# Performance work log

Hardware: AMD Instinct MI355X
Metric: run time of the kernel (lower is better)

Reference implementation:

```python
import jax, jax.numpy as jnp
import numpy as np

B, L, D, NLAYERS, MAX_NODES, DEG = 32, 512, 768, 3, 128, 8


def _build_graph():
    rng = np.random.default_rng(0)
    per = rng.integers(-32, 33, size=B // 2)
    sizes = np.concatenate([96 + per, 96 - per]).astype(np.int64)  # sum = 96*B = 3072, each in [64,128]
    N = int(sizes.sum())
    offs = np.concatenate([[0], np.cumsum(sizes)])
    batch = np.repeat(np.arange(B), sizes).astype(np.int64)
    pad_idx = np.zeros((B, MAX_NODES), np.int64)
    pad_mask = np.zeros((B, MAX_NODES), bool)
    src, dst = [], []
    for b in range(B):
        n = int(sizes[b])
        pad_idx[b, :n] = np.arange(offs[b], offs[b] + n)
        pad_mask[b, :n] = True
        src.append(rng.integers(offs[b], offs[b] + n, n * DEG))
        dst.append(rng.integers(offs[b], offs[b] + n, n * DEG))
    return N, batch, pad_idx, pad_mask, np.concatenate(src), np.concatenate(dst)


def setup_inputs() -> dict:
    N, batch, pad_idx, pad_mask, esrc, edst = _build_graph()
    key = jax.random.key(0)
    ks = jax.random.split(key, 8)
    s = 1.0 / np.sqrt(D)
    return {
        "x": jax.random.normal(ks[0], (N, D), jnp.float32),
        "text": jax.random.normal(ks[1], (B, L, D), jnp.float32),
        "batch_ent1_d_mask": jnp.ones((B, 1), jnp.float32),
        "batch_ent1_g_mask": jnp.ones((B, 1), jnp.float32),
        "gnn_ws": jax.random.normal(ks[2], (NLAYERS, D, D), jnp.float32) * s,
        "gnn_wn": jax.random.normal(ks[3], (NLAYERS, D, D), jnp.float32) * s,
        "gnn_b": jnp.zeros((NLAYERS, D), jnp.float32),
        "atom_w": jax.random.normal(ks[4], (D, D), jnp.float32) * s,
        "atom_b": jnp.zeros((D,), jnp.float32),
        "rand_emb": jax.random.normal(ks[5], (1, D), jnp.float32),
        "batch": jnp.asarray(batch),
        "pad_idx": jnp.asarray(pad_idx),
        "pad_mask": jnp.asarray(pad_mask),
        "edge_src": jnp.asarray(esrc),
        "edge_dst": jnp.asarray(edst),
    }


def reference(x, text, batch_ent1_d_mask, batch_ent1_g_mask, gnn_ws, gnn_wn, gnn_b,
              atom_w, atom_b, rand_emb, batch, pad_idx, pad_mask, edge_src, edge_dst):
    N = x.shape[0]
    E = edge_src.shape[0]
    maskf = pad_mask.astype(x.dtype)            # [B, M]
    n_per = maskf.sum(axis=1)                   # [B] num real nodes per graph
    # edge-neighbor mean counts (constants w.r.t. x)
    cnt = jax.ops.segment_sum(jnp.ones((E,), x.dtype), edge_dst, num_segments=N)
    inv_cnt = 1.0 / jnp.maximum(cnt, 1.0)
    cms = []
    for i in range(NLAYERS):
        # MoleGraphConv stand-in: mean neighbor aggregation + self transform
        msg = jax.ops.segment_sum(x[edge_src], edge_dst, num_segments=N) * inv_cnt[:, None]
        x = jax.nn.relu(x @ gnn_ws[i] + msg @ gnn_wn[i] + gnn_b[i])
        # ragged gather into padded [B, M, D]
        xp = x[pad_idx] * maskf[..., None]
        # graph -> text cross attention (softmax over text tokens; no mask needed)
        g2t = jax.nn.softmax(jnp.einsum('bmd,bld->bml', xp, text), axis=-1)
        g2t_out = jnp.einsum('bml,bld->bmd', g2t, text)            # [B, M, D]
        # text -> graph cross attention (mask padded nodes)
        t2g_logits = jnp.einsum('bld,bmd->blm', text, xp)
        t2g_logits = jnp.where(pad_mask[:, None, :], t2g_logits, jnp.float32(-1e9))
        t2g = jax.nn.softmax(t2g_logits, axis=-1)
        t2g_out = jnp.einsum('blm,bmd->bld', t2g, xp)              # [B, L, D]
        # mean over concatenated rows [n_i + L] per graph (pool_type=2)
        pooled = ((g2t_out * maskf[..., None]).sum(axis=1) + t2g_out.sum(axis=1)) \
                 / (n_per + jnp.float32(L))[:, None]
        cms.append(pooled)
    out_cms = jnp.mean(jnp.stack(cms, axis=1), axis=1)              # mean over layers
    out_t = text[:, 0, :]
    # scatter-mean of final node features per graph
    gsum = jax.ops.segment_sum(x, batch, num_segments=B)
    gcnt = jax.ops.segment_sum(jnp.ones((N,), x.dtype), batch, num_segments=B)
    xg = gsum / jnp.maximum(gcnt, 1.0)[:, None]
    # dropout is a no-op in eval mode
    out_g = jnp.tanh(xg @ atom_w + atom_b)
    z = rand_emb[0]
    dg = batch_ent1_d_mask * batch_ent1_g_mask
    return jnp.concatenate([
        out_t * batch_ent1_d_mask + (1 - batch_ent1_d_mask) * z,
        out_g * batch_ent1_g_mask + (1 - batch_ent1_g_mask) * z,
        out_cms * dg + (1 - dg) * z,
    ], axis=-1)
```

## Files before the change

### kernel.cpp

```cpp
#include <hip/hip_runtime.h>

#define D 768
#define B 32
#define L 512
#define M 128
#define NNODES 3072
#define NEDGES 24576

using bf16x8 = __attribute__((ext_vector_type(8))) short;
using f32x4  = __attribute__((ext_vector_type(4))) float;

__device__ __forceinline__ float bf2f(unsigned short u) {
  union { unsigned int i; float f; } v; v.i = ((unsigned int)u) << 16; return v.f;
}
__device__ __forceinline__ unsigned short f2bf(float f) {
  union { float f; unsigned int i; } v; v.f = f;
  unsigned int x = v.i;
  return (unsigned short)((x + 0x7FFFu + ((x >> 16) & 1u)) >> 16);
}
__device__ __forceinline__ float ldf(const void* p, size_t i, int f32) {
  return f32 ? ((const float*)p)[i] : bf2f(((const unsigned short*)p)[i]);
}
__device__ __forceinline__ int ldi(const void* p, size_t i, int w64) {
  return w64 ? (int)((const long long*)p)[i] : ((const int*)p)[i];
}
__device__ __forceinline__ f32x4 mfma16(bf16x8 a, bf16x8 b, f32x4 c) {
  return __builtin_amdgcn_mfma_f32_16x16x32_bf16(a, b, c, 0, 0, 0);
}
__device__ __forceinline__ void gl_lds(const unsigned short* gsrc, unsigned short* lbase,
                                       int lane) {
  __builtin_amdgcn_global_load_lds(
      (const __attribute__((address_space(1))) unsigned int*)(gsrc + lane * 8),
      (__attribute__((address_space(3))) unsigned int*)lbase, 16, 0, 0);
}

__device__ __forceinline__ float pk_read(const unsigned short* P, int p, int l, int d) {
  return bf2f(P[(((size_t)(p * 24 + (d >> 5))) << 9) + ((((d & 31) >> 3) << 4) + l) * 8 + (d & 7)]);
}


__global__ void k_init(int* cnt, int* cursor, int* gcnt, float* pooled,
                       const unsigned short* __restrict__ t,
                       const unsigned int* __restrict__ e, int* __restrict__ flags) {
  int i = blockIdx.x * 256 + threadIdx.x;
  if (i < NNODES) { cnt[i] = 0; cursor[i] = 0; }
  if (i < B) gcnt[i] = 0;
  if (i < B * D) pooled[i] = 0.f;
  if (blockIdx.x == 0) {
    __shared__ int r0[256];
    __shared__ unsigned r1[256];
    int tid = threadIdx.x;
    int bad = 0;
    for (int j = tid; j < 8192; j += 256) {
      unsigned short u = t[2 * j];
      unsigned ex = (u >> 7) & 0xFF;
      if (ex >= 0xC0) bad = 1;
    }
    unsigned o = 0;
    for (int j = tid; j < NEDGES / 2; j += 256) o |= e[2 * j + 1];
    r0[tid] = bad; r1[tid] = o;
    __syncthreads();
    for (int s = 128; s > 0; s >>= 1) {
      if (tid < s) { r0[tid] |= r0[tid + s]; r1[tid] |= r1[tid + s]; }
      __syncthreads();
    }
    if (tid == 0) { flags[0] = r0[0]; flags[1] = (r1[0] == 0) ? 1 : 0; }
  }
}

__global__ __launch_bounds__(256) void k_pack_in(
    const void* __restrict__ x_in, unsigned short* __restrict__ x0,
    unsigned short* __restrict__ PkA, const void* __restrict__ text,
    unsigned short* __restrict__ Tpk, const int* __restrict__ flags) {
  __shared__ unsigned short buf[12288];
  int f = flags[0];
  int bid = blockIdx.x, tid = threadIdx.x;
  const void* src; unsigned short* dst; unsigned short* rows; int p;
  if (bid < NNODES / 16) { src = x_in; dst = PkA; rows = x0; p = bid; }
  else                   { src = text; dst = Tpk; rows = nullptr; p = bid - NNODES / 16; }
#pragma unroll
  for (int j = 0; j < 6; ++j) {
    int idx = j * 256 + tid;
    int r = idx / 96, c = idx % 96;
    size_t sbase = (size_t)(p * 16 + r) * 768 + c * 8;
    union { unsigned short v[8]; uint4 q; } u;
    if (f) {
      const float* sp = (const float*)src + sbase;
#pragma unroll
      for (int e = 0; e < 8; ++e) u.v[e] = f2bf(sp[e]);
    } else {
      const unsigned short* sp = (const unsigned short*)src + sbase;
#pragma unroll
      for (int e = 0; e < 8; ++e) u.v[e] = sp[e];
    }
    if (rows) *(uint4*)&rows[sbase] = u.q;
    int lpos = (c >> 2) * 64 + (c & 3) * 16 + r;
#pragma unroll
    for (int e = 0; e < 8; ++e) buf[lpos * 8 + e] = u.v[e];
  }
  __syncthreads();
  uint4* d4 = (uint4*)(dst + (size_t)p * 12288);
  const uint4* b4 = (const uint4*)buf;
#pragma unroll
  for (int j = 0; j < 6; ++j) d4[j * 256 + tid] = b4[j * 256 + tid];
}

__global__ __launch_bounds__(256) void k_pack(const unsigned short* __restrict__ src,
                                              unsigned short* __restrict__ dst) {
  __shared__ unsigned short buf[12288];
  int p = blockIdx.x, tid = threadIdx.x;
#pragma unroll
  for (int j = 0; j < 6; ++j) {
    int idx = j * 256 + tid;
    int r = idx / 96, c = idx % 96;
    size_t sbase = (size_t)(p * 16 + r) * 768 + c * 8;
    uint4 q = *(const uint4*)(src + sbase);
    int lpos = (c >> 2) * 64 + (c & 3) * 16 + r;
    *(uint4*)&buf[lpos * 8] = q;
  }
  __syncthreads();
  uint4* d4 = (uint4*)(dst + (size_t)p * 12288);
  const uint4* b4 = (const uint4*)buf;
#pragma unroll
  for (int j = 0; j < 6; ++j) d4[j * 256 + tid] = b4[j * 256 + tid];
}

__global__ void k_count(const void* __restrict__ edst, const void* __restrict__ batch,
                        const int* __restrict__ flags, int* __restrict__ cnt,
                        int* __restrict__ gcnt) {
  int w = flags[1];
  int i = blockIdx.x * 256 + threadIdx.x;
  if (i < NEDGES) atomicAdd(&cnt[ldi(edst, i, w)], 1);
  if (i < NNODES) atomicAdd(&gcnt[ldi(batch, i, w)], 1);
}

__global__ void k_scan(const int* __restrict__ cnt, int* __restrict__ rowstart) {
  __shared__ int a[NNODES], b[NNODES];
  int tid = threadIdx.x;
  for (int i = tid; i < NNODES; i += 1024) a[i] = cnt[i];
  __syncthreads();
  int* s = a; int* d = b;
  for (int off = 1; off < NNODES; off <<= 1) {
    for (int i = tid; i < NNODES; i += 1024)
      d[i] = s[i] + (i >= off ? s[i - off] : 0);
    __syncthreads();
    int* t = s; s = d; d = t;
  }
  for (int i = tid; i < NNODES; i += 1024) rowstart[i + 1] = s[i];
  if (tid == 0) rowstart[0] = 0;
}

__global__ void k_scatter(const void* __restrict__ esrc, const void* __restrict__ edst,
                          const int* __restrict__ flags, const int* __restrict__ rowstart,
                          int* __restrict__ cursor, int* __restrict__ csr) {
  int w = flags[1];
  int i = blockIdx.x * 256 + threadIdx.x;
  if (i < NEDGES) {
    int dd = ldi(edst, i, w);
    int pos = atomicAdd(&cursor[dd], 1);
    csr[rowstart[dd] + pos] = ldi(esrc, i, w);
  }
}

__global__ void k_transpose(const void* __restrict__ Ws, const void* __restrict__ Wn,
                            const void* __restrict__ Aw, const int* __restrict__ flags,
                            unsigned short* __restrict__ WsT,
                            unsigned short* __restrict__ WnT,
                            unsigned short* __restrict__ AwT) {
  __shared__ unsigned short tile[32][33];
  int f = flags[0];
  int z = blockIdx.z;
  const void* src; unsigned short* dst; size_t zoff;
  if (z < 3)      { src = Ws; zoff = (size_t)z * D * D;       dst = WsT + zoff; }
  else if (z < 6) { src = Wn; zoff = (size_t)(z - 3) * D * D; dst = WnT + zoff; }
  else            { src = Aw; zoff = 0;                       dst = AwT; }
  int k0 = blockIdx.x * 32, n0 = blockIdx.y * 32;
  int tx = threadIdx.x, ty = threadIdx.y;
#pragma unroll
  for (int j = 0; j < 4; ++j)
    tile[ty + j * 8][tx] = f2bf(ldf(src, zoff + (size_t)(k0 + ty + j * 8) * D + n0 + tx, f));
  __syncthreads();
#pragma unroll
  for (int j = 0; j < 4; ++j)
    dst[(size_t)(n0 + ty + j * 8) * D + k0 + tx] = tile[tx][ty + j * 8];
}

__global__ __launch_bounds__(256) void k_packw(
    const unsigned short* __restrict__ WsT, const unsigned short* __restrict__ WnT,
    const unsigned short* __restrict__ AwT, unsigned short* __restrict__ WsPk,
    unsigned short* __restrict__ WnPk, unsigned short* __restrict__ AwPk) {
  __shared__ unsigned short buf[12288];
  int z = blockIdx.y;
  const unsigned short* src; unsigned short* dst;
  if (z < 3)      { src = WsT + (size_t)z * D * D;       dst = WsPk + (size_t)z * D * D; }
  else if (z < 6) { src = WnT + (size_t)(z - 3) * D * D; dst = WnPk + (size_t)(z - 3) * D * D; }
  else            { src = AwT;                           dst = AwPk; }
  int p = blockIdx.x, tid = threadIdx.x;
#pragma unroll
  for (int j = 0; j < 6; ++j) {
    int idx = j * 256 + tid;
    int r = idx / 96, c = idx % 96;
    size_t sbase = (size_t)(p * 16 + r) * 768 + c * 8;
    uint4 q = *(const uint4*)(src + sbase);
    int lpos = (c >> 2) * 64 + (c & 3) * 16 + r;
    *(uint4*)&buf[lpos * 8] = q;
  }
  __syncthreads();
  uint4* d4 = (uint4*)(dst + (size_t)p * 12288);
  const uint4* b4 = (const uint4*)buf;
#pragma unroll
  for (int j = 0; j < 6; ++j) d4[j * 256 + tid] = b4[j * 256 + tid];
}


__global__ __launch_bounds__(256) void k_msg_pack(
    const unsigned short* __restrict__ x, const int* __restrict__ cnt,
    const int* __restrict__ rowstart, const int* __restrict__ csr,
    unsigned short* __restrict__ Mpk) {
  __shared__ unsigned short buf[12288];
  int p = blockIdx.x, tid = threadIdx.x;
  int w = tid >> 6, lane = tid & 63;
#pragma unroll
  for (int i = 0; i < 4; ++i) {
    int r = w * 4 + i;
    int n = p * 16 + r;
    int deg = cnt[n], base = rowstart[n];
    float inv = 1.0f / (float)(deg > 1 ? deg : 1);
    float a[12];
#pragma unroll
    for (int j = 0; j < 12; ++j) a[j] = 0.f;
    for (int e = 0; e < deg; ++e) {
      const uint2* xr = (const uint2*)(x + (size_t)csr[base + e] * D);
#pragma unroll
      for (int j = 0; j < 3; ++j) {
        uint2 v = xr[lane + j * 64];
        a[j * 4 + 0] += bf2f((unsigned short)(v.x & 0xFFFFu));
        a[j * 4 + 1] += bf2f((unsigned short)(v.x >> 16));
        a[j * 4 + 2] += bf2f((unsigned short)(v.y & 0xFFFFu));
        a[j * 4 + 3] += bf2f((unsigned short)(v.y >> 16));
      }
    }
#pragma unroll
    for (int j = 0; j < 3; ++j) {
      int d0 = (lane + j * 64) * 4;
      int c = d0 >> 3, e0 = d0 & 7;
      int lpos = (c >> 2) * 64 + (c & 3) * 16 + r;
      unsigned short* bp = &buf[lpos * 8 + e0];
      bp[0] = f2bf(a[j * 4 + 0] * inv);
      bp[1] = f2bf(a[j * 4 + 1] * inv);
      bp[2] = f2bf(a[j * 4 + 2] * inv);
      bp[3] = f2bf(a[j * 4 + 3] * inv);
    }
  }
  __syncthreads();
  uint4* d4 = (uint4*)(Mpk + (size_t)p * 12288);
  const uint4* b4 = (const uint4*)buf;
#pragma unroll
  for (int j = 0; j < 6; ++j) d4[j * 256 + tid] = b4[j * 256 + tid];
}

__global__ __launch_bounds__(256) void k_gemm_gnn(
    const unsigned short* __restrict__ Xpk, const unsigned short* __restrict__ Mpk,
    const unsigned short* __restrict__ WsPk, const unsigned short* __restrict__ WnPk,
    const void* __restrict__ bias, size_t bias_off, const int* __restrict__ flags,
    unsigned short* __restrict__ Y) {
  __shared__ __align__(16) unsigned short lds[2][4096];
  int f = flags[0];
  int tid = threadIdx.x;
  int wave = tid >> 6, lane = tid & 63;
  int q = lane >> 4, t = lane & 15;
  int wm = wave >> 1, wn = wave & 1;
  int pa = blockIdx.x * 4, pb = blockIdx.y * 4;
  f32x4 acc[2][2];
#pragma unroll
  for (int mi = 0; mi < 2; ++mi)
#pragma unroll
    for (int ni = 0; ni < 2; ++ni)
      acc[mi][ni] = (f32x4){0.f, 0.f, 0.f, 0.f};

  int c0 = wave * 2;
  for (int r = 0; r < 24; ++r) {
    int s0 = r * 2;
    int h = (s0 < 24) ? 0 : 1;
    int kk0 = s0 - h * 24;
    const unsigned short* P = (wave < 2) ? (h ? Mpk : Xpk) : (h ? WnPk : WsPk);
    int pan0 = (wave < 2) ? (pa + c0) : (pb + c0 - 4);
    gl_lds(P + (((size_t)(pan0 * 24 + kk0)) << 9), &lds[0][c0 * 512], lane);
    gl_lds(P + (((size_t)((pan0 + 1) * 24 + kk0)) << 9), &lds[0][(c0 + 1) * 512], lane);
    gl_lds(P + (((size_t)(pan0 * 24 + kk0 + 1)) << 9), &lds[1][c0 * 512], lane);
    gl_lds(P + (((size_t)((pan0 + 1) * 24 + kk0 + 1)) << 9), &lds[1][(c0 + 1) * 512], lane);
    __syncthreads();
#pragma unroll
    for (int st = 0; st < 2; ++st) {
      bf16x8 a0 = *(const bf16x8*)&lds[st][(wm * 2 + 0) * 512 + lane * 8];
      bf16x8 a1 = *(const bf16x8*)&lds[st][(wm * 2 + 1) * 512 + lane * 8];
      bf16x8 b0 = *(const bf16x8*)&lds[st][(4 + wn * 2 + 0) * 512 + lane * 8];
      bf16x8 b1 = *(const bf16x8*)&lds[st][(4 + wn * 2 + 1) * 512 + lane * 8];
      acc[0][0] = mfma16(a0, b0, acc[0][0]);
      acc[0][1] = mfma16(a0, b1, acc[0][1]);
      acc[1][0] = mfma16(a1, b0, acc[1][0]);
      acc[1][1] = mfma16(a1, b1, acc[1][1]);
    }
    __syncthreads();
  }

#pragma unroll
  for (int ni = 0; ni < 2; ++ni) {
    int col = blockIdx.y * 64 + wn * 32 + ni * 16 + t;
    float bv = ldf(bias, bias_off + col, f);
#pragma unroll
    for (int mi = 0; mi < 2; ++mi) {
#pragma unroll
      for (int r = 0; r < 4; ++r) {
        int row = blockIdx.x * 64 + wm * 32 + mi * 16 + q * 4 + r;
        float v = acc[mi][ni][r] + bv;
        Y[(size_t)row * D + col] = f2bf(v > 0.f ? v : 0.f);
      }
    }
  }
}

__global__ __launch_bounds__(256) void k_xp_pack(
    const unsigned short* __restrict__ Xn, const void* __restrict__ pidx,
    const int* __restrict__ flags, const int* __restrict__ gcnt,
    unsigned short* __restrict__ xp, unsigned short* __restrict__ XpPk) {
  __shared__ unsigned short rows[16 * 776];
  int p = blockIdx.x, tid = threadIdx.x;
  int w64 = flags[1];
  int r = tid >> 4, c16 = tid & 15;
  int bm = p * 16 + r;
  int b = bm >> 7, m = bm & 127;
  int nb = gcnt[b];
  uint4* dl = (uint4*)&rows[r * 776];
  if (m < nb) {
    const uint4* srcr = (const uint4*)(Xn + (size_t)ldi(pidx, bm, w64) * D);
#pragma unroll
    for (int j = 0; j < 6; ++j) dl[c16 + j * 16] = srcr[c16 + j * 16];
  } else {
    uint4 z = {0u, 0u, 0u, 0u};
#pragma unroll
    for (int j = 0; j < 6; ++j) dl[c16 + j * 16] = z;
  }
  __syncthreads();
#pragma unroll
  for (int j = 0; j < 6; ++j) {
    int idx = j * 256 + tid;
    int rr = idx / 96, cc = idx % 96;
    uint4 vv = *(const uint4*)&rows[rr * 776 + cc * 8];
    *(uint4*)&xp[(size_t)(p * 16 + rr) * D + cc * 8] = vv;
  }
  unsigned short* pb = XpPk + (size_t)p * 12288;
#pragma unroll
  for (int j = 0; j < 6; ++j) {
    int odx = j * 256 + tid;
    int kk = odx >> 6, lanep = odx & 63;
    int rr = lanep & 15, cg = lanep >> 4;
    int cc = kk * 4 + cg;
    uint4 vv = *(const uint4*)&rows[rr * 776 + cc * 8];
    *(uint4*)&pb[odx * 8] = vv;
  }
}

__global__ __launch_bounds__(256) void k_scores(
    const unsigned short* __restrict__ XpPk, const unsigned short* __restrict__ Tpk,
    float* __restrict__ S) {
  __shared__ __align__(16) unsigned short lds[2][4096];
  int b = blockIdx.z;
  int tid = threadIdx.x;
  int wave = tid >> 6, lane = tid & 63;
  int q = lane >> 4, t = lane & 15;
  int wm = wave >> 1, wn = wave & 1;
  int pa = b * 8 + blockIdx.x * 4;
  int pb = b * 32 + blockIdx.y * 4;
  f32x4 acc[2][2];
#pragma unroll
  for (int mi = 0; mi < 2; ++mi)
#pragma unroll
    for (int ni = 0; ni < 2; ++ni)
      acc[mi][ni] = (f32x4){0.f, 0.f, 0.f, 0.f};

  int c0 = wave * 2;
  const unsigned short* P = (wave < 2) ? XpPk : Tpk;
  int pan0 = (wave < 2) ? (pa + c0) : (pb + c0 - 4);
  for (int r = 0; r < 12; ++r) {
    int s0 = r * 2;
    gl_lds(P + (((size_t)(pan0 * 24 + s0)) << 9), &lds[0][c0 * 512], lane);
    gl_lds(P + (((size_t)((pan0 + 1) * 24 + s0)) << 9), &lds[0][(c0 + 1) * 512], lane);
    gl_lds(P + (((size_t)(pan0 * 24 + s0 + 1)) << 9), &lds[1][c0 * 512], lane);
    gl_lds(P + (((size_t)((pan0 + 1) * 24 + s0 + 1)) << 9), &lds[1][(c0 + 1) * 512], lane);
    __syncthreads();
#pragma unroll
    for (int st = 0; st < 2; ++st) {
      bf16x8 a0 = *(const bf16x8*)&lds[st][(wm * 2 + 0) * 512 + lane * 8];
      bf16x8 a1 = *(const bf16x8*)&lds[st][(wm * 2 + 1) * 512 + lane * 8];
      bf16x8 b0 = *(const bf16x8*)&lds[st][(4 + wn * 2 + 0) * 512 + lane * 8];
      bf16x8 b1 = *(const bf16x8*)&lds[st][(4 + wn * 2 + 1) * 512 + lane * 8];
      acc[0][0] = mfma16(a0, b0, acc[0][0]);
      acc[0][1] = mfma16(a0, b1, acc[0][1]);
      acc[1][0] = mfma16(a1, b0, acc[1][0]);
      acc[1][1] = mfma16(a1, b1, acc[1][1]);
    }
    __syncthreads();
  }

  float* Sb = S + (size_t)b * M * L;
#pragma unroll
  for (int ni = 0; ni < 2; ++ni) {
    int col = blockIdx.y * 64 + wn * 32 + ni * 16 + t;
#pragma unroll
    for (int mi = 0; mi < 2; ++mi) {
#pragma unroll
      for (int r = 0; r < 4; ++r) {
        int row = blockIdx.x * 64 + wm * 32 + mi * 16 + q * 4 + r;
        Sb[(size_t)row * L + col] = acc[mi][ni][r];
      }
    }
  }
}

__global__ __launch_bounds__(256) void k_stats(
    const float* __restrict__ S, const int* __restrict__ gcnt,
    float* __restrict__ rmax, float* __restrict__ rsum,
    float* __restrict__ cmaxv, float* __restrict__ csumv) {
  int bid = blockIdx.x, tid = threadIdx.x;
  if (bid < B * M) {
    __shared__ float red[4];
    int lane = tid & 63, wv = tid >> 6;
    const float* r = S + (size_t)bid * L;
    float s0 = r[tid], s1 = r[tid + 256];
    float m = fmaxf(s0, s1);
#pragma unroll
    for (int o = 32; o > 0; o >>= 1) m = fmaxf(m, __shfl_down(m, o));
    if (lane == 0) red[wv] = m;
    __syncthreads();
    float bm = fmaxf(fmaxf(red[0], red[1]), fmaxf(red[2], red[3]));
    __syncthreads();
    float e = __expf(s0 - bm) + __expf(s1 - bm);
#pragma unroll
    for (int o = 32; o > 0; o >>= 1) e += __shfl_down(e, o);
    if (lane == 0) red[wv] = e;
    __syncthreads();
    if (tid == 0) { rmax[bid] = bm; rsum[bid] = red[0] + red[1] + red[2] + red[3]; }
  } else {
    __shared__ float pm[4][64], ps[4][64];
    int cid = bid - B * M;
    int b = cid >> 3, ly = cid & 7;
    int w = tid >> 6, lane = tid & 63;
    int l = ly * 64 + lane;
    int nb = gcnt[b];
    const float* Sb = S + (size_t)b * M * L;
    int m0 = w * 32, m1 = min(m0 + 32, nb);
    float cm = -1e30f, cs = 0.f;
    for (int m = m0; m < m1; ++m) {
      float s = Sb[(size_t)m * L + l];
      if (s > cm) { cs = cs * __expf(cm - s) + 1.f; cm = s; }
      else cs += __expf(s - cm);
    }
    pm[w][lane] = cm; ps[w][lane] = cs;
    __syncthreads();
    if (w == 0) {
      float CM = -1e30f;
#pragma unroll
      for (int j = 0; j < 4; ++j) CM = fmaxf(CM, pm[j][lane]);
      float CS = 0.f;
#pragma unroll
      for (int j = 0; j < 4; ++j) CS += ps[j][lane] * __expf(pm[j][lane] - CM);
      cmaxv[b * L + l] = CM; csumv[b * L + l] = CS;
    }
  }
}

__global__ __launch_bounds__(256) void k_cross(
    const float* __restrict__ S, const float* __restrict__ rmax,
    const float* __restrict__ rsum, const float* __restrict__ cmaxv,
    const float* __restrict__ csumv, const int* __restrict__ gcnt,
    float* __restrict__ wv, float* __restrict__ t2gcol) {
  int bid = blockIdx.x, tid = threadIdx.x;
  if (bid < 256) {
    __shared__ float rm[M], ri[M];
    __shared__ float pw[4][64];
    int b = bid >> 3, ly = bid & 7;
    int w = tid >> 6, lane = tid & 63;
    if (tid < M) { rm[tid] = rmax[b * M + tid]; ri[tid] = 1.f / rsum[b * M + tid]; }
    __syncthreads();
    int l = ly * 64 + lane;
    int nb = gcnt[b];
    const float* Sb = S + (size_t)b * M * L;
    int m0 = w * 32, m1 = min(m0 + 32, nb);
    float wp = 0.f;
    for (int m = m0; m < m1; ++m)
      wp += __expf(Sb[(size_t)m * L + l] - rm[m]) * ri[m];
    pw[w][lane] = wp;
    __syncthreads();
    if (w == 0)
      wv[b * L + l] = pw[0][lane] + pw[1][lane] + pw[2][lane] + pw[3][lane];
  } else {
    __shared__ float red[4];
    int bm = bid - 256;
    int b = bm >> 7, m = bm & 127;
    int lane = tid & 63, w = tid >> 6;
    int nb = gcnt[b];
    float acc = 0.f;
    if (m < nb) {
      const float* r = S + (size_t)bm * L;
      const float* cm = cmaxv + b * L;
      const float* cs = csumv + b * L;
      acc = __expf(r[tid] - cm[tid]) / cs[tid]
          + __expf(r[tid + 256] - cm[tid + 256]) / cs[tid + 256];
    }
#pragma unroll
    for (int o = 32; o > 0; o >>= 1) acc += __shfl_down(acc, o);
    if (lane == 0) red[w] = acc;
    __syncthreads();
    if (tid == 0) t2gcol[bm] = red[0] + red[1] + red[2] + red[3];
  }
}

__global__ __launch_bounds__(256) void k_pooled(
    const float* __restrict__ wv, const float* __restrict__ t2gcol,
    const unsigned short* __restrict__ Tpk, const unsigned short* __restrict__ xp,
    const int* __restrict__ gcnt, float* __restrict__ pooled) {
  int b = blockIdx.x;
  int d = blockIdx.y * 256 + threadIdx.x;
  int c = blockIdx.z;
  float acc = 0.f;
  if (c < 8) {
    int l0 = c * 64;
    for (int l = l0; l < l0 + 64; ++l) {
      int p = b * 32 + (l >> 4);
      acc += wv[b * L + l] * pk_read(Tpk, p, l & 15, d);
    }
  } else {
    const unsigned short* Xb = xp + (size_t)b * M * D;
    int mm0 = (c - 8) * 64;
    for (int m = mm0; m < mm0 + 64; ++m) acc += t2gcol[b * M + m] * bf2f(Xb[(size_t)m * D + d]);
  }
  atomicAdd(&pooled[(size_t)b * D + d], acc / ((float)gcnt[b] + 512.f));
}


__global__ __launch_bounds__(256) void k_xg(const unsigned short* __restrict__ xp,
                                            const int* __restrict__ gcnt,
                                            unsigned short* __restrict__ xgb) {
  int b = blockIdx.x;
  int d = blockIdx.y * 256 + threadIdx.x;
  int nb = gcnt[b];
  float inv = 1.0f / (float)(nb > 1 ? nb : 1);
  const unsigned short* Xb = xp + (size_t)b * M * D;
  float s = 0.f;
  for (int m = 0; m < M; ++m) s += bf2f(Xb[(size_t)m * D + d]);
  xgb[(size_t)b * D + d] = f2bf(s * inv);
}

__global__ __launch_bounds__(256) void k_atom(const unsigned short* __restrict__ xgb,
                                              const unsigned short* __restrict__ AwPk,
                                              float* __restrict__ gpre) {
  int tid = threadIdx.x;
  int w = tid >> 6, lane = tid & 63;
  int q = lane >> 4, t = lane & 15;
  int nbase = blockIdx.x * 64 + w * 16;
  int pb = nbase >> 4;
  f32x4 acc[2];
  acc[0] = (f32x4){0.f, 0.f, 0.f, 0.f};
  acc[1] = (f32x4){0.f, 0.f, 0.f, 0.f};
  for (int kk = 0; kk < 24; ++kk) {
    bf16x8 a0 = *(const bf16x8*)(xgb + (size_t)t * D + kk * 32 + q * 8);
    bf16x8 a1 = *(const bf16x8*)(xgb + (size_t)(16 + t) * D + kk * 32 + q * 8);
    bf16x8 bv = *(const bf16x8*)(AwPk + (((size_t)(pb * 24 + kk)) << 9) + (lane << 3));
    acc[0] = mfma16(a0, bv, acc[0]);
    acc[1] = mfma16(a1, bv, acc[1]);
  }
#pragma unroll
  for (int mi = 0; mi < 2; ++mi)
#pragma unroll
    for (int r = 0; r < 4; ++r) {
      int row = mi * 16 + q * 4 + r;
      gpre[(size_t)row * D + nbase + t] = acc[mi][r];
    }
}

__global__ __launch_bounds__(256) void k_final(
    const unsigned short* __restrict__ Tpk, const float* __restrict__ gpre,
    const float* __restrict__ pooled, const void* __restrict__ ab,
    const void* __restrict__ dmask, const void* __restrict__ gmask,
    const void* __restrict__ remb, const int* __restrict__ flags,
    void* __restrict__ out) {
  int f = flags[0];
  int b = blockIdx.x, tid = threadIdx.x;
  float dm = ldf(dmask, b, f);
  float gm = ldf(gmask, b, f);
  float dg = dm * gm;
  size_t base = (size_t)b * 2304;
#pragma unroll
  for (int j = 0; j < 3; ++j) {
    int d = tid + j * 256;
    float z = ldf(remb, d, f);
    float tv = pk_read(Tpk, b * 32, 0, d);
    float o0 = tv * dm + (1.f - dm) * z;
    float gv = tanhf(gpre[(size_t)b * D + d] + ldf(ab, d, f));
    float o1 = gv * gm + (1.f - gm) * z;
    float p = pooled[(size_t)b * D + d] * (1.f / 3.f);
    float o2 = p * dg + (1.f - dg) * z;
    if (f) {
      float* of = (float*)out;
      of[base + d] = o0; of[base + 768 + d] = o1; of[base + 1536 + d] = o2;
    } else {
      unsigned short* ob = (unsigned short*)out;
      ob[base + d] = f2bf(o0); ob[base + 768 + d] = f2bf(o1); ob[base + 1536 + d] = f2bf(o2);
    }
  }
}

extern "C" void kernel_launch(void* const* d_in, const int* in_sizes, int n_in,
                              void* d_out, int out_size, void* d_ws, size_t ws_size,
                              hipStream_t stream) {
  const void* x_in  = d_in[0];
  const void* text  = d_in[1];
  const void* dmask = d_in[2];
  const void* gmask = d_in[3];
  const void* gws   = d_in[4];
  const void* gwn   = d_in[5];
  const void* gb    = d_in[6];
  const void* aw    = d_in[7];
  const void* ab    = d_in[8];
  const void* remb  = d_in[9];
  const void* batch = d_in[10];
  const void* pidx  = d_in[11];
  const void* esrc  = d_in[13];
  const void* edst  = d_in[14];

  char* wsp = (char*)d_ws;
  size_t off = 0;
  auto carve = [&](size_t bytes) -> void* {
    void* p = wsp + off;
    off += (bytes + 255) & ~(size_t)255;
    return p;
  };
  int* flags = (int*)carve(2 * 4);
  unsigned short* x0    = (unsigned short*)carve((size_t)NNODES * D * 2);
  unsigned short* xA    = (unsigned short*)carve((size_t)NNODES * D * 2);
  unsigned short* xB    = (unsigned short*)carve((size_t)NNODES * D * 2);
  unsigned short* PkA   = (unsigned short*)carve((size_t)NNODES * D * 2);
  unsigned short* PkB   = (unsigned short*)carve((size_t)NNODES * D * 2);
  unsigned short* Mpk   = (unsigned short*)carve((size_t)NNODES * D * 2);
  unsigned short* Tpk   = (unsigned short*)carve((size_t)B * L * D * 2);
  unsigned short* WsT   = (unsigned short*)carve((size_t)3 * D * D * 2);
  unsigned short* WnT   = (unsigned short*)carve((size_t)3 * D * D * 2);
  unsigned short* AwT   = (unsigned short*)carve((size_t)D * D * 2);
  unsigned short* WsPk  = (unsigned short*)carve((size_t)3 * D * D * 2);
  unsigned short* WnPk  = (unsigned short*)carve((size_t)3 * D * D * 2);
  unsigned short* AwPk  = (unsigned short*)carve((size_t)D * D * 2);
  unsigned short* xp    = (unsigned short*)carve((size_t)B * M * D * 2);
  unsigned short* XpPk  = (unsigned short*)carve((size_t)B * M * D * 2);
  unsigned short* xgb   = (unsigned short*)carve((size_t)B * D * 2);
  float* gpre    = (float*)carve((size_t)B * D * 4);
  float* S       = (float*)carve((size_t)B * M * L * 4);
  float* rmax    = (float*)carve((size_t)B * M * 4);
  float* rsum    = (float*)carve((size_t)B * M * 4);
  float* wv      = (float*)carve((size_t)B * L * 4);
  float* cmaxv   = (float*)carve((size_t)B * L * 4);
  float* csumv   = (float*)carve((size_t)B * L * 4);
  float* t2gcol  = (float*)carve((size_t)B * M * 4);
  float* pooled  = (float*)carve((size_t)B * D * 4);
  int* cnt      = (int*)carve((size_t)NNODES * 4);
  int* rowstart = (int*)carve((size_t)(NNODES + 1) * 4);
  int* cursor   = (int*)carve((size_t)NNODES * 4);
  int* gcnt     = (int*)carve((size_t)B * 4);
  int* csr      = (int*)carve((size_t)NEDGES * 4);

  k_init<<<96, 256, 0, stream>>>(cnt, cursor, gcnt, pooled,
                                 (const unsigned short*)text, (const unsigned int*)edst, flags);
  k_pack_in<<<NNODES / 16 + B * L / 16, 256, 0, stream>>>(x_in, x0, PkA, text, Tpk, flags);
  k_transpose<<<dim3(24, 24, 7), dim3(32, 8), 0, stream>>>(gws, gwn, aw, flags, WsT, WnT, AwT);
  k_packw<<<dim3(48, 7), 256, 0, stream>>>(WsT, WnT, AwT, WsPk, WnPk, AwPk);
  k_count<<<96, 256, 0, stream>>>(edst, batch, flags, cnt, gcnt);
  k_scan<<<1, 1024, 0, stream>>>(cnt, rowstart);
  k_scatter<<<96, 256, 0, stream>>>(esrc, edst, flags, rowstart, cursor, csr);

  const unsigned short* xsrc = x0;
  const unsigned short* Apk = PkA;
  unsigned short* Y[3]   = {xA, xB, xA};
  unsigned short* Npk[3] = {PkB, PkA, nullptr};
  for (int i = 0; i < 3; ++i) {
    k_msg_pack<<<NNODES / 16, 256, 0, stream>>>(xsrc, cnt, rowstart, csr, Mpk);
    k_gemm_gnn<<<dim3(48, 12), 256, 0, stream>>>(Apk, Mpk, WsPk + (size_t)i * D * D,
                                                 WnPk + (size_t)i * D * D, gb, (size_t)i * D,
                                                 flags, Y[i]);
    if (i < 2) k_pack<<<NNODES / 16, 256, 0, stream>>>(Y[i], Npk[i]);
    k_xp_pack<<<B * M / 16, 256, 0, stream>>>(Y[i], pidx, flags, gcnt, xp, XpPk);
    k_scores<<<dim3(2, 8, B), 256, 0, stream>>>(XpPk, Tpk, S);
    k_stats<<<B * M + 256, 256, 0, stream>>>(S, gcnt, rmax, rsum, cmaxv, csumv);
    k_cross<<<256 + B * M, 256, 0, stream>>>(S, rmax, rsum, cmaxv, csumv, gcnt, wv, t2gcol);
    k_pooled<<<dim3(B, 3, 10), 256, 0, stream>>>(wv, t2gcol, Tpk, xp, gcnt, pooled);
    xsrc = Y[i];
    Apk = Npk[i];
  }
  k_xg<<<dim3(B, 3), 256, 0, stream>>>(xp, gcnt, xgb);
  k_atom<<<12, 256, 0, stream>>>(xgb, AwPk, gpre);
  k_final<<<B, 256, 0, stream>>>(Tpk, gpre, pooled, ab, dmask, gmask, remb, flags, d_out);
}
```

Measured before the change: 487.5 us.

## Fuse weight transpose+pack, deepen GEMM K-staging, fold graph mean into xp_pack

```diff
diff --git a/kernel.cpp b/kernel.cpp
--- a/kernel.cpp
+++ b/kernel.cpp
@@ -39,13 +39,13 @@
 }
 
 
-__global__ void k_init(int* cnt, int* cursor, int* gcnt, float* pooled,
+__global__ void k_init(int* cnt, int* cursor, int* gcnt, float* pooled, float* xgacc,
                        const unsigned short* __restrict__ t,
                        const unsigned int* __restrict__ e, int* __restrict__ flags) {
   int i = blockIdx.x * 256 + threadIdx.x;
   if (i < NNODES) { cnt[i] = 0; cursor[i] = 0; }
   if (i < B) gcnt[i] = 0;
-  if (i < B * D) pooled[i] = 0.f;
+  if (i < B * D) { pooled[i] = 0.f; xgacc[i] = 0.f; }
   if (blockIdx.x == 0) {
     __shared__ int r0[256];
     __shared__ unsigned r1[256];
@@ -125,6 +125,46 @@
   for (int j = 0; j < 6; ++j) d4[j * 256 + tid] = b4[j * 256 + tid];
 }
 
+__global__ __launch_bounds__(256) void k_wpack(
+    const void* __restrict__ Ws, const void* __restrict__ Wn, const void* __restrict__ Aw,
+    const int* __restrict__ flags, unsigned short* __restrict__ WsPk,
+    unsigned short* __restrict__ WnPk, unsigned short* __restrict__ AwPk) {
+  __shared__ unsigned short buf[2048];
+  int f = flags[0];
+  int z = blockIdx.z;
+  const void* src; unsigned short* dst; size_t zoff;
+  if (z < 3)      { src = Ws; zoff = (size_t)z * D * D;       dst = WsPk + zoff; }
+  else if (z < 6) { src = Wn; zoff = (size_t)(z - 3) * D * D; dst = WnPk + zoff; }
+  else            { src = Aw; zoff = 0;                       dst = AwPk; }
+  int n0 = blockIdx.x * 64, kk = blockIdx.y;
+  int tid = threadIdx.x;
+  int kl = tid >> 3, c8 = tid & 7;
+  size_t sbase = zoff + (size_t)(kk * 32 + kl) * D + n0 + c8 * 8;
+  unsigned short v[8];
+  if (f) {
+    const float* sp = (const float*)src + sbase;
+#pragma unroll
+    for (int e = 0; e < 8; ++e) v[e] = f2bf(sp[e]);
+  } else {
+    const unsigned short* sp = (const unsigned short*)src + sbase;
+#pragma unroll
+    for (int e = 0; e < 8; ++e) v[e] = sp[e];
+  }
+  int ebit = kl & 7, quad = kl >> 3;
+#pragma unroll
+  for (int i = 0; i < 8; ++i) {
+    int nl = c8 * 8 + i;
+    int pl = nl >> 4;
+    int lane = quad * 16 + (nl & 15);
+    buf[pl * 512 + lane * 8 + ebit] = v[i];
+  }
+  __syncthreads();
+  int pl = tid >> 6, pos = tid & 63;
+  int pG = blockIdx.x * 4 + pl;
+  uint4 q = *(const uint4*)&buf[pl * 512 + pos * 8];
+  *(uint4*)&dst[(((size_t)(pG * 24 + kk)) << 9) + pos * 8] = q;
+}
+
 __global__ void k_count(const void* __restrict__ edst, const void* __restrict__ batch,
                         const int* __restrict__ flags, int* __restrict__ cnt,
                         int* __restrict__ gcnt) {
@@ -162,56 +202,6 @@
   }
 }
 
-__global__ void k_transpose(const void* __restrict__ Ws, const void* __restrict__ Wn,
-                            const void* __restrict__ Aw, const int* __restrict__ flags,
-                            unsigned short* __restrict__ WsT,
-                            unsigned short* __restrict__ WnT,
-                            unsigned short* __restrict__ AwT) {
-  __shared__ unsigned short tile[32][33];
-  int f = flags[0];
-  int z = blockIdx.z;
-  const void* src; unsigned short* dst; size_t zoff;
-  if (z < 3)      { src = Ws; zoff = (size_t)z * D * D;       dst = WsT + zoff; }
-  else if (z < 6) { src = Wn; zoff = (size_t)(z - 3) * D * D; dst = WnT + zoff; }
-  else            { src = Aw; zoff = 0;                       dst = AwT; }
-  int k0 = blockIdx.x * 32, n0 = blockIdx.y * 32;
-  int tx = threadIdx.x, ty = threadIdx.y;
-#pragma unroll
-  for (int j = 0; j < 4; ++j)
-    tile[ty + j * 8][tx] = f2bf(ldf(src, zoff + (size_t)(k0 + ty + j * 8) * D + n0 + tx, f));
-  __syncthreads();
-#pragma unroll
-  for (int j = 0; j < 4; ++j)
-    dst[(size_t)(n0 + ty + j * 8) * D + k0 + tx] = tile[tx][ty + j * 8];
-}
-
-__global__ __launch_bounds__(256) void k_packw(
-    const unsigned short* __restrict__ WsT, const unsigned short* __restrict__ WnT,
-    const unsigned short* __restrict__ AwT, unsigned short* __restrict__ WsPk,
-    unsigned short* __restrict__ WnPk, unsigned short* __restrict__ AwPk) {
-  __shared__ unsigned short buf[12288];
-  int z = blockIdx.y;
-  const unsigned short* src; unsigned short* dst;
-  if (z < 3)      { src = WsT + (size_t)z * D * D;       dst = WsPk + (size_t)z * D * D; }
-  else if (z < 6) { src = WnT + (size_t)(z - 3) * D * D; dst = WnPk + (size_t)(z - 3) * D * D; }
-  else            { src = AwT;                           dst = AwPk; }
-  int p = blockIdx.x, tid = threadIdx.x;
-#pragma unroll
-  for (int j = 0; j < 6; ++j) {
-    int idx = j * 256 + tid;
-    int r = idx / 96, c = idx % 96;
-    size_t sbase = (size_t)(p * 16 + r) * 768 + c * 8;
-    uint4 q = *(const uint4*)(src + sbase);
-    int lpos = (c >> 2) * 64 + (c & 3) * 16 + r;
-    *(uint4*)&buf[lpos * 8] = q;
-  }
-  __syncthreads();
-  uint4* d4 = (uint4*)(dst + (size_t)p * 12288);
-  const uint4* b4 = (const uint4*)buf;
-#pragma unroll
-  for (int j = 0; j < 6; ++j) d4[j * 256 + tid] = b4[j * 256 + tid];
-}
-
 
 __global__ __launch_bounds__(256) void k_msg_pack(
     const unsigned short* __restrict__ x, const int* __restrict__ cnt,
@@ -264,7 +254,7 @@
     const unsigned short* __restrict__ WsPk, const unsigned short* __restrict__ WnPk,
     const void* __restrict__ bias, size_t bias_off, const int* __restrict__ flags,
     unsigned short* __restrict__ Y) {
-  __shared__ __align__(16) unsigned short lds[2][4096];
+  __shared__ __align__(16) unsigned short lds[6 * 4096];
   int f = flags[0];
   int tid = threadIdx.x;
   int wave = tid >> 6, lane = tid & 63;
@@ -279,23 +269,23 @@
       acc[mi][ni] = (f32x4){0.f, 0.f, 0.f, 0.f};
 
   int c0 = wave * 2;
-  for (int r = 0; r < 24; ++r) {
-    int s0 = r * 2;
-    int h = (s0 < 24) ? 0 : 1;
-    int kk0 = s0 - h * 24;
+  int pan0A = (wave < 2) ? (pa + c0) : (pb + c0 - 4);
+  for (int r = 0; r < 8; ++r) {
+    int h = r >> 2;
+    int kk0 = r * 6 - h * 24;
     const unsigned short* P = (wave < 2) ? (h ? Mpk : Xpk) : (h ? WnPk : WsPk);
-    int pan0 = (wave < 2) ? (pa + c0) : (pb + c0 - 4);
-    gl_lds(P + (((size_t)(pan0 * 24 + kk0)) << 9), &lds[0][c0 * 512], lane);
-    gl_lds(P + (((size_t)((pan0 + 1) * 24 + kk0)) << 9), &lds[0][(c0 + 1) * 512], lane);
-    gl_lds(P + (((size_t)(pan0 * 24 + kk0 + 1)) << 9), &lds[1][c0 * 512], lane);
-    gl_lds(P + (((size_t)((pan0 + 1) * 24 + kk0 + 1)) << 9), &lds[1][(c0 + 1) * 512], lane);
-    __syncthreads();
-#pragma unroll
-    for (int st = 0; st < 2; ++st) {
-      bf16x8 a0 = *(const bf16x8*)&lds[st][(wm * 2 + 0) * 512 + lane * 8];
-      bf16x8 a1 = *(const bf16x8*)&lds[st][(wm * 2 + 1) * 512 + lane * 8];
-      bf16x8 b0 = *(const bf16x8*)&lds[st][(4 + wn * 2 + 0) * 512 + lane * 8];
-      bf16x8 b1 = *(const bf16x8*)&lds[st][(4 + wn * 2 + 1) * 512 + lane * 8];
+#pragma unroll
+    for (int st = 0; st < 6; ++st) {
+      gl_lds(P + (((size_t)(pan0A * 24 + kk0 + st)) << 9), &lds[st * 4096 + c0 * 512], lane);
+      gl_lds(P + (((size_t)((pan0A + 1) * 24 + kk0 + st)) << 9), &lds[st * 4096 + (c0 + 1) * 512], lane);
+    }
+    __syncthreads();
+#pragma unroll
+    for (int st = 0; st < 6; ++st) {
+      bf16x8 a0 = *(const bf16x8*)&lds[st * 4096 + (wm * 2 + 0) * 512 + lane * 8];
+      bf16x8 a1 = *(const bf16x8*)&lds[st * 4096 + (wm * 2 + 1) * 512 + lane * 8];
+      bf16x8 b0 = *(const bf16x8*)&lds[st * 4096 + (4 + wn * 2 + 0) * 512 + lane * 8];
+      bf16x8 b1 = *(const bf16x8*)&lds[st * 4096 + (4 + wn * 2 + 1) * 512 + lane * 8];
       acc[0][0] = mfma16(a0, b0, acc[0][0]);
       acc[0][1] = mfma16(a0, b1, acc[0][1]);
       acc[1][0] = mfma16(a1, b0, acc[1][0]);
@@ -323,7 +313,8 @@
 __global__ __launch_bounds__(256) void k_xp_pack(
     const unsigned short* __restrict__ Xn, const void* __restrict__ pidx,
     const int* __restrict__ flags, const int* __restrict__ gcnt,
-    unsigned short* __restrict__ xp, unsigned short* __restrict__ XpPk) {
+    unsigned short* __restrict__ xp, unsigned short* __restrict__ XpPk,
+    float* __restrict__ xgacc) {
   __shared__ unsigned short rows[16 * 776];
   int p = blockIdx.x, tid = threadIdx.x;
   int w64 = flags[1];
@@ -359,12 +350,23 @@
     uint4 vv = *(const uint4*)&rows[rr * 776 + cc * 8];
     *(uint4*)&pb[odx * 8] = vv;
   }
+  if (xgacc) {
+    int bb = p >> 3;
+#pragma unroll
+    for (int j = 0; j < 3; ++j) {
+      int d = j * 256 + tid;
+      float s = 0.f;
+#pragma unroll
+      for (int rr = 0; rr < 16; ++rr) s += bf2f(rows[rr * 776 + d]);
+      atomicAdd(&xgacc[(size_t)bb * D + d], s);
+    }
+  }
 }
 
 __global__ __launch_bounds__(256) void k_scores(
     const unsigned short* __restrict__ XpPk, const unsigned short* __restrict__ Tpk,
     float* __restrict__ S) {
-  __shared__ __align__(16) unsigned short lds[2][4096];
+  __shared__ __align__(16) unsigned short lds[6 * 4096];
   int b = blockIdx.z;
   int tid = threadIdx.x;
   int wave = tid >> 6, lane = tid & 63;
@@ -382,19 +384,20 @@
   int c0 = wave * 2;
   const unsigned short* P = (wave < 2) ? XpPk : Tpk;
   int pan0 = (wave < 2) ? (pa + c0) : (pb + c0 - 4);
-  for (int r = 0; r < 12; ++r) {
-    int s0 = r * 2;
-    gl_lds(P + (((size_t)(pan0 * 24 + s0)) << 9), &lds[0][c0 * 512], lane);
-    gl_lds(P + (((size_t)((pan0 + 1) * 24 + s0)) << 9), &lds[0][(c0 + 1) * 512], lane);
-    gl_lds(P + (((size_t)(pan0 * 24 + s0 + 1)) << 9), &lds[1][c0 * 512], lane);
-    gl_lds(P + (((size_t)((pan0 + 1) * 24 + s0 + 1)) << 9), &lds[1][(c0 + 1) * 512], lane);
-    __syncthreads();
-#pragma unroll
-    for (int st = 0; st < 2; ++st) {
-      bf16x8 a0 = *(const bf16x8*)&lds[st][(wm * 2 + 0) * 512 + lane * 8];
-      bf16x8 a1 = *(const bf16x8*)&lds[st][(wm * 2 + 1) * 512 + lane * 8];
-      bf16x8 b0 = *(const bf16x8*)&lds[st][(4 + wn * 2 + 0) * 512 + lane * 8];
-      bf16x8 b1 = *(const bf16x8*)&lds[st][(4 + wn * 2 + 1) * 512 + lane * 8];
+  for (int r = 0; r < 4; ++r) {
+    int kk0 = r * 6;
+#pragma unroll
+    for (int st = 0; st < 6; ++st) {
+      gl_lds(P + (((size_t)(pan0 * 24 + kk0 + st)) << 9), &lds[st * 4096 + c0 * 512], lane);
+      gl_lds(P + (((size_t)((pan0 + 1) * 24 + kk0 + st)) << 9), &lds[st * 4096 + (c0 + 1) * 512], lane);
+    }
+    __syncthreads();
+#pragma unroll
+    for (int st = 0; st < 6; ++st) {
+      bf16x8 a0 = *(const bf16x8*)&lds[st * 4096 + (wm * 2 + 0) * 512 + lane * 8];
+      bf16x8 a1 = *(const bf16x8*)&lds[st * 4096 + (wm * 2 + 1) * 512 + lane * 8];
+      bf16x8 b0 = *(const bf16x8*)&lds[st * 4096 + (4 + wn * 2 + 0) * 512 + lane * 8];
+      bf16x8 b1 = *(const bf16x8*)&lds[st * 4096 + (4 + wn * 2 + 1) * 512 + lane * 8];
       acc[0][0] = mfma16(a0, b0, acc[0][0]);
       acc[0][1] = mfma16(a0, b1, acc[0][1]);
       acc[1][0] = mfma16(a1, b0, acc[1][0]);
@@ -539,20 +542,8 @@
 }
 
 
-__global__ __launch_bounds__(256) void k_xg(const unsigned short* __restrict__ xp,
-                                            const int* __restrict__ gcnt,
-                                            unsigned short* __restrict__ xgb) {
-  int b = blockIdx.x;
-  int d = blockIdx.y * 256 + threadIdx.x;
-  int nb = gcnt[b];
-  float inv = 1.0f / (float)(nb > 1 ? nb : 1);
-  const unsigned short* Xb = xp + (size_t)b * M * D;
-  float s = 0.f;
-  for (int m = 0; m < M; ++m) s += bf2f(Xb[(size_t)m * D + d]);
-  xgb[(size_t)b * D + d] = f2bf(s * inv);
-}
-
-__global__ __launch_bounds__(256) void k_atom(const unsigned short* __restrict__ xgb,
+__global__ __launch_bounds__(256) void k_atom(const float* __restrict__ xgacc,
+                                              const int* __restrict__ gcnt,
                                               const unsigned short* __restrict__ AwPk,
                                               float* __restrict__ gpre) {
   int tid = threadIdx.x;
@@ -560,15 +551,21 @@
   int q = lane >> 4, t = lane & 15;
   int nbase = blockIdx.x * 64 + w * 16;
   int pb = nbase >> 4;
+  int n0 = gcnt[t], n1 = gcnt[16 + t];
+  float inv0 = 1.f / (float)(n0 > 1 ? n0 : 1);
+  float inv1 = 1.f / (float)(n1 > 1 ? n1 : 1);
   f32x4 acc[2];
   acc[0] = (f32x4){0.f, 0.f, 0.f, 0.f};
   acc[1] = (f32x4){0.f, 0.f, 0.f, 0.f};
   for (int kk = 0; kk < 24; ++kk) {
-    bf16x8 a0 = *(const bf16x8*)(xgb + (size_t)t * D + kk * 32 + q * 8);
-    bf16x8 a1 = *(const bf16x8*)(xgb + (size_t)(16 + t) * D + kk * 32 + q * 8);
+    const float* s0 = xgacc + (size_t)t * D + kk * 32 + q * 8;
+    const float* s1 = xgacc + (size_t)(16 + t) * D + kk * 32 + q * 8;
+    union { unsigned short v[8]; bf16x8 f; } a0, a1;
+#pragma unroll
+    for (int j = 0; j < 8; ++j) { a0.v[j] = f2bf(s0[j] * inv0); a1.v[j] = f2bf(s1[j] * inv1); }
     bf16x8 bv = *(const bf16x8*)(AwPk + (((size_t)(pb * 24 + kk)) << 9) + (lane << 3));
-    acc[0] = mfma16(a0, bv, acc[0]);
-    acc[1] = mfma16(a1, bv, acc[1]);
+    acc[0] = mfma16(a0.f, bv, acc[0]);
+    acc[1] = mfma16(a1.f, bv, acc[1]);
   }
 #pragma unroll
   for (int mi = 0; mi < 2; ++mi)
@@ -644,15 +641,12 @@
   unsigned short* PkB   = (unsigned short*)carve((size_t)NNODES * D * 2);
   unsigned short* Mpk   = (unsigned short*)carve((size_t)NNODES * D * 2);
   unsigned short* Tpk   = (unsigned short*)carve((size_t)B * L * D * 2);
-  unsigned short* WsT   = (unsigned short*)carve((size_t)3 * D * D * 2);
-  unsigned short* WnT   = (unsigned short*)carve((size_t)3 * D * D * 2);
-  unsigned short* AwT   = (unsigned short*)carve((size_t)D * D * 2);
   unsigned short* WsPk  = (unsigned short*)carve((size_t)3 * D * D * 2);
   unsigned short* WnPk  = (unsigned short*)carve((size_t)3 * D * D * 2);
   unsigned short* AwPk  = (unsigned short*)carve((size_t)D * D * 2);
   unsigned short* xp    = (unsigned short*)carve((size_t)B * M * D * 2);
   unsigned short* XpPk  = (unsigned short*)carve((size_t)B * M * D * 2);
-  unsigned short* xgb   = (unsigned short*)carve((size_t)B * D * 2);
+  float* xgacc   = (float*)carve((size_t)B * D * 4);
   float* gpre    = (float*)carve((size_t)B * D * 4);
   float* S       = (float*)carve((size_t)B * M * L * 4);
   float* rmax    = (float*)carve((size_t)B * M * 4);
@@ -668,11 +662,10 @@
   int* gcnt     = (int*)carve((size_t)B * 4);
   int* csr      = (int*)carve((size_t)NEDGES * 4);
 
-  k_init<<<96, 256, 0, stream>>>(cnt, cursor, gcnt, pooled,
+  k_init<<<96, 256, 0, stream>>>(cnt, cursor, gcnt, pooled, xgacc,
                                  (const unsigned short*)text, (const unsigned int*)edst, flags);
   k_pack_in<<<NNODES / 16 + B * L / 16, 256, 0, stream>>>(x_in, x0, PkA, text, Tpk, flags);
-  k_transpose<<<dim3(24, 24, 7), dim3(32, 8), 0, stream>>>(gws, gwn, aw, flags, WsT, WnT, AwT);
-  k_packw<<<dim3(48, 7), 256, 0, stream>>>(WsT, WnT, AwT, WsPk, WnPk, AwPk);
+  k_wpack<<<dim3(12, 24, 7), 256, 0, stream>>>(gws, gwn, aw, flags, WsPk, WnPk, AwPk);
   k_count<<<96, 256, 0, stream>>>(edst, batch, flags, cnt, gcnt);
   k_scan<<<1, 1024, 0, stream>>>(cnt, rowstart);
   k_scatter<<<96, 256, 0, stream>>>(esrc, edst, flags, rowstart, cursor, csr);
@@ -687,7 +680,8 @@
                                                  WnPk + (size_t)i * D * D, gb, (size_t)i * D,
                                                  flags, Y[i]);
     if (i < 2) k_pack<<<NNODES / 16, 256, 0, stream>>>(Y[i], Npk[i]);
-    k_xp_pack<<<B * M / 16, 256, 0, stream>>>(Y[i], pidx, flags, gcnt, xp, XpPk);
+    k_xp_pack<<<B * M / 16, 256, 0, stream>>>(Y[i], pidx, flags, gcnt, xp, XpPk,
+                                              (i == 2) ? xgacc : nullptr);
     k_scores<<<dim3(2, 8, B), 256, 0, stream>>>(XpPk, Tpk, S);
     k_stats<<<B * M + 256, 256, 0, stream>>>(S, gcnt, rmax, rsum, cmaxv, csumv);
     k_cross<<<256 + B * M, 256, 0, stream>>>(S, rmax, rsum, cmaxv, csumv, gcnt, wv, t2gcol);
@@ -695,7 +689,6 @@
     xsrc = Y[i];
     Apk = Npk[i];
   }
-  k_xg<<<dim3(B, 3), 256, 0, stream>>>(xp, gcnt, xgb);
-  k_atom<<<12, 256, 0, stream>>>(xgb, AwPk, gpre);
+  k_atom<<<12, 256, 0, stream>>>(xgacc, gcnt, AwPk, gpre);
   k_final<<<B, 256, 0, stream>>>(Tpk, gpre, pooled, ab, dmask, gmask, remb, flags, d_out);
 }
```

After: 471.2 us. -3.3%, faster.
